# Optimization experiments

Measured on AMD Instinct MI355X. Metric: run time of the kernel, lower is better.

Reference implementation:

```python
import jax, jax.numpy as jnp
import numpy as np
from jax import lax

B, N, C_IN = 8, 4096, 64
NPOINT, NSAMPLE, RADIUS = 1024, 32, 0.2
BN_EPS = 1e-3  # keras BatchNormalization default epsilon


def _fps(pts):
    """Farthest point sampling on a single cloud pts: (N, 3) -> (NPOINT,) int32."""
    n = pts.shape[0]
    def step(carry, _):
        dist, far = carry
        c = pts[far]                                  # (3,)
        d = jnp.sum((pts - c) ** 2, axis=-1)          # (N,)
        dist = jnp.minimum(dist, d)
        nxt = jnp.argmax(dist).astype(jnp.int32)
        return (dist, nxt), far
    init = (jnp.full((n,), 1e10, pts.dtype), jnp.array(0, jnp.int32))
    _, idx = lax.scan(step, init, None, length=NPOINT)
    return idx


def _ball_query(xyz, new_xyz):
    """xyz: (B,N,3), new_xyz: (B,P,3) -> idx (B,P,NSAMPLE) int32.
    First NSAMPLE point indices within RADIUS of each centroid (in original
    order); slots beyond the in-ball count are filled with the first in-ball
    index, matching the PointNet++ CUDA query_ball_point semantics."""
    n = xyz.shape[1]
    # squared distances via the expansion trick to avoid a (B,P,N,3) temp
    d2 = (jnp.sum(new_xyz ** 2, -1)[:, :, None]
          + jnp.sum(xyz ** 2, -1)[:, None, :]
          - 2.0 * jnp.einsum('bpc,bnc->bpn', new_xyz, xyz))  # (B,P,N)
    in_ball = d2 < RADIUS ** 2
    cand = jnp.where(in_ball, jnp.arange(n, dtype=jnp.int32)[None, None, :], n)
    neg_top, _ = lax.top_k(-cand, NSAMPLE)   # NSAMPLE smallest indices
    idx = -neg_top                           # ascending order
    first = idx[..., :1]                     # centroid itself is always in-ball
    idx = jnp.where(idx == n, first, idx)
    return idx


def _group(feats, idx):
    """feats: (B,N,C), idx: (B,P,S) -> (B,P,S,C) gather per batch."""
    return jax.vmap(lambda f, i: f[i])(feats, idx)


def _mlp_layer(x, W, g, b, m, v):
    # 1x1 conv (no bias) + BN (inference stats) + ReLU
    x = jnp.einsum('bpsc,cd->bpsd', x, W)
    x = (x - m) * lax.rsqrt(v + BN_EPS) * g + b
    return jax.nn.relu(x)


def setup_inputs() -> dict:
    key = jax.random.key(0)
    ks = jax.random.split(key, 8)
    xyz = jax.random.uniform(ks[0], (B, N, 3), dtype=jnp.float32)
    points = jax.random.normal(ks[1], (B, N, C_IN), dtype=jnp.float32)
    c0 = 3 + C_IN  # use_xyz=True
    W0 = jax.random.normal(ks[2], (c0, 64), jnp.float32) / np.sqrt(c0)
    W1 = jax.random.normal(ks[3], (64, 64), jnp.float32) / np.sqrt(64.0)
    W2 = jax.random.normal(ks[4], (64, 128), jnp.float32) / np.sqrt(64.0)
    def bn(c):
        return (jnp.ones((c,), jnp.float32), jnp.zeros((c,), jnp.float32),
                jnp.zeros((c,), jnp.float32), jnp.ones((c,), jnp.float32))
    g0, b0, m0, v0 = bn(64)
    g1, b1, m1, v1 = bn(64)
    g2, b2, m2, v2 = bn(128)
    return dict(xyz=xyz, points=points,
                W0=W0, g0=g0, b0=b0, m0=m0, v0=v0,
                W1=W1, g1=g1, b1=b1, m1=m1, v1=v1,
                W2=W2, g2=g2, b2=b2, m2=m2, v2=v2)


def reference(xyz, points,
              W0, g0, b0, m0, v0,
              W1, g1, b1, m1, v1,
              W2, g2, b2, m2, v2):
    # --- sample_and_group ---
    fps_idx = jax.vmap(_fps)(xyz)                            # (B,P)
    new_xyz = jnp.take_along_axis(xyz, fps_idx[:, :, None], axis=1)  # (B,P,3)
    idx = _ball_query(xyz, new_xyz)                          # (B,P,S)
    grouped_xyz = _group(xyz, idx) - new_xyz[:, :, None, :]  # (B,P,S,3)
    grouped_pts = _group(points, idx)                        # (B,P,S,C)
    new_points = jnp.concatenate([grouped_xyz, grouped_pts], axis=-1)
    # --- shared per-point MLP (1x1 conv + BN + ReLU) ---
    new_points = _mlp_layer(new_points, W0, g0, b0, m0, v0)
    new_points = _mlp_layer(new_points, W1, g1, b1, m1, v1)
    new_points = _mlp_layer(new_points, W2, g2, b2, m2, v2)
    # --- max pool over the neighborhood axis ---
    new_points = jnp.max(new_points, axis=2)                 # (B,P,128)
    return new_xyz, new_points, idx
```

## Files before the change

kernel.cpp:

```cpp
#include <hip/hip_runtime.h>
#include <stdint.h>

#define BN_EPS 0.001f

typedef float v2f __attribute__((ext_vector_type(2)));

__global__ __launch_bounds__(256) void fps_kernel(const float* __restrict__ xyz,
                                                  float* __restrict__ new_xyz) {
#pragma clang fp contract(off)
  __shared__ float px[4096], py[4096], pz[4096];
  __shared__ unsigned long long wk[2][4];
  __shared__ int curh[1024];
  const int b = blockIdx.x;
  const int t = threadIdx.x;
  const int lane = t & 63, wid = t >> 6;
  const float* X = xyz + (size_t)b * 4096 * 3;
  v2f x[8], y[8], z[8], dist[8];
#pragma unroll
  for (int j = 0; j < 8; ++j) {
    const int n0 = (2 * j) * 256 + t;
    const int n1 = (2 * j + 1) * 256 + t;
    x[j].x = X[n0 * 3 + 0]; x[j].y = X[n1 * 3 + 0];
    y[j].x = X[n0 * 3 + 1]; y[j].y = X[n1 * 3 + 1];
    z[j].x = X[n0 * 3 + 2]; z[j].y = X[n1 * 3 + 2];
    px[n0] = x[j].x; py[n0] = y[j].x; pz[n0] = z[j].x;
    px[n1] = x[j].y; py[n1] = y[j].y; pz[n1] = z[j].y;
    dist[j] = (v2f){1e10f, 1e10f};
  }
  __syncthreads();
  int cur = 0;
  for (int it = 0; it < 1024; ++it) {
    if (t == 0) curh[it] = cur;
    const float cx = px[cur], cy = py[cur], cz = pz[cur];
    const v2f cxv = {cx, cx}, cyv = {cy, cy}, czv = {cz, cz};
    float bestv = -1.0f;
    int bestj = 0;
#pragma unroll
    for (int j = 0; j < 8; ++j) {
      v2f dx = x[j] - cxv, dy = y[j] - cyv, dz = z[j] - czv;
      v2f d = dx * dx + dy * dy;
      d = d + dz * dz;
      v2f nd = __builtin_elementwise_min(dist[j], d);
      dist[j] = nd;
      if (nd.x > bestv) { bestv = nd.x; bestj = 2 * j; }
      if (nd.y > bestv) { bestv = nd.y; bestj = 2 * j + 1; }
    }
    const int besti = bestj * 256 + t;
    unsigned long long key =
        ((unsigned long long)__float_as_uint(bestv) << 32) | (unsigned)(~besti);
#define DPP_STEP(CTRL)                                                                     \
    {                                                                                      \
      unsigned lo_ = (unsigned)key, hi_ = (unsigned)(key >> 32);                           \
      unsigned ls = (unsigned)__builtin_amdgcn_update_dpp((int)lo_, (int)lo_, CTRL, 0xf, 0xf, false); \
      unsigned hs = (unsigned)__builtin_amdgcn_update_dpp((int)hi_, (int)hi_, CTRL, 0xf, 0xf, false); \
      unsigned long long sk = ((unsigned long long)hs << 32) | ls;                         \
      if (sk > key) key = sk;                                                              \
    }
    DPP_STEP(0x111)
    DPP_STEP(0x112)
    DPP_STEP(0x114)
    DPP_STEP(0x118)
    DPP_STEP(0x142)
    DPP_STEP(0x143)
#undef DPP_STEP
    const unsigned whi = (unsigned)__builtin_amdgcn_readlane((int)(key >> 32), 63);
    const unsigned wlo = (unsigned)__builtin_amdgcn_readlane((int)key, 63);
    if (lane == 0) wk[it & 1][wid] = ((unsigned long long)whi << 32) | wlo;
    __syncthreads();
    const unsigned long long k0 = wk[it & 1][0], k1 = wk[it & 1][1];
    const unsigned long long k2 = wk[it & 1][2], k3 = wk[it & 1][3];
    unsigned long long b01 = (k1 > k0) ? k1 : k0;
    unsigned long long b23 = (k3 > k2) ? k3 : k2;
    unsigned long long bk = (b23 > b01) ? b23 : b01;
    cur = (int)(~(unsigned)(bk & 0xffffffffull));
  }
  __syncthreads();
  float* out = new_xyz + (size_t)b * 1024 * 3;
  for (int it = t; it < 1024; it += 256) {
    const int c = curh[it];
    out[it * 3 + 0] = px[c];
    out[it * 3 + 1] = py[c];
    out[it * 3 + 2] = pz[c];
  }
}

__global__ __launch_bounds__(256) void ballq_kernel(const float* __restrict__ xyz,
                                                    const float* __restrict__ new_xyz,
                                                    float* __restrict__ idxf) {
#pragma clang fp contract(off)
  const int wv = threadIdx.x >> 6, lane = threadIdx.x & 63;
  const int pg = blockIdx.x * 4 + wv;
  const int b = pg >> 10;
  const float* X = xyz + (size_t)b * 4096 * 3;
  const float cx = new_xyz[pg * 3 + 0];
  const float cy = new_xyz[pg * 3 + 1];
  const float cz = new_xyz[pg * 3 + 2];
  const float csq = (cx * cx + cy * cy) + cz * cz;
  float* out = idxf + (size_t)pg * 32;
  int total = 0;
  int first = -1;
  for (int chunk = 0; chunk < 64; ++chunk) {
    const int n = chunk * 64 + lane;
    const float xx = X[n * 3 + 0], yy = X[n * 3 + 1], zz = X[n * 3 + 2];
    const float sq = (xx * xx + yy * yy) + zz * zz;
    const float dot = fmaf(cz, zz, fmaf(cy, yy, cx * xx));
    const float d2 = (csq + sq) - 2.0f * dot;
    const bool in = d2 < 0.04f;
    const unsigned long long mask = __ballot(in);
    if (first < 0 && mask != 0ull) first = chunk * 64 + __builtin_ctzll(mask);
    if (in) {
      const int pos = total + __builtin_popcountll(mask & ((1ull << lane) - 1ull));
      if (pos < 32) out[pos] = (float)n;
    }
    total += __builtin_popcountll(mask);
    if (total >= 32) break;
  }
  if (total < 32 && first >= 0) {
    const int slot = total + lane;
    if (slot < 32) out[slot] = (float)first;
  }
}

__global__ __launch_bounds__(256) void mlp_kernel(
    const float* __restrict__ xyz, const float* __restrict__ points,
    const float* __restrict__ new_xyz, const float* __restrict__ idxf,
    const float* __restrict__ W0, const float* __restrict__ g0,
    const float* __restrict__ b0, const float* __restrict__ m0,
    const float* __restrict__ v0, const float* __restrict__ W1,
    const float* __restrict__ g1, const float* __restrict__ b1,
    const float* __restrict__ m1, const float* __restrict__ v1,
    const float* __restrict__ W2, const float* __restrict__ g2,
    const float* __restrict__ b2, const float* __restrict__ m2,
    const float* __restrict__ v2, float* __restrict__ new_points) {
  __shared__ __align__(16) float W0s[67 * 64];
  __shared__ __align__(16) float W1s[64 * 64];
  __shared__ __align__(16) float sh[64 * 36];
  __shared__ __align__(16) float h0T[64 * 34];
  __shared__ float s0c[64], t0c[64], s1c[64], t1c[64], s2c[128], t2c[128];
  const int t = threadIdx.x;
  float* inT = sh;
  float* h1T = sh;

  for (int i = t; i < 67 * 64; i += 256) W0s[i] = W0[i];
  for (int i = t; i < 64 * 64; i += 256) W1s[i] = W1[i];
  if (t < 64) {
    float s = g0[t] * rsqrtf(v0[t] + BN_EPS); s0c[t] = s; t0c[t] = b0[t] - m0[t] * s;
    float u = g1[t] * rsqrtf(v1[t] + BN_EPS); s1c[t] = u; t1c[t] = b1[t] - m1[t] * u;
  }
  if (t < 128) {
    float s = g2[t] * rsqrtf(v2[t] + BN_EPS); s2c[t] = s; t2c[t] = b2[t] - m2[t] * s;
  }
  __syncthreads();

  const int sgrp = t & 15, dgrp = t >> 4;
  const int dg2 = t & 31, sg2 = t >> 5;
  float* pmax = h0T;

  for (int pp = 0; pp < 4; ++pp) {
    const int pg = blockIdx.x * 4 + pp;
    const int b = pg >> 10;
    const float cx = new_xyz[pg * 3 + 0];
    const float cy = new_xyz[pg * 3 + 1];
    const float cz = new_xyz[pg * 3 + 2];
    {
      const int s = t >> 3, cg = t & 7;
      const int i = (int)idxf[(size_t)pg * 32 + s];
      const float* Pr = points + ((size_t)b * 4096 + i) * 64 + cg * 8;
      const float4 a = *(const float4*)Pr;
      const float4 c4 = *(const float4*)(Pr + 4);
      const int r = 3 + cg * 8;
      inT[(r + 0) * 34 + s] = a.x;  inT[(r + 1) * 34 + s] = a.y;
      inT[(r + 2) * 34 + s] = a.z;  inT[(r + 3) * 34 + s] = a.w;
      inT[(r + 4) * 34 + s] = c4.x; inT[(r + 5) * 34 + s] = c4.y;
      inT[(r + 6) * 34 + s] = c4.z; inT[(r + 7) * 34 + s] = c4.w;
      if (t < 32) {
        const int i2 = (int)idxf[(size_t)pg * 32 + t];
        const float* Xr = xyz + ((size_t)b * 4096 + i2) * 3;
        inT[0 * 34 + t] = Xr[0] - cx;
        inT[1 * 34 + t] = Xr[1] - cy;
        inT[2 * 34 + t] = Xr[2] - cz;
      }
    }
    __syncthreads();
    {
      float acc[2][4] = {{0, 0, 0, 0}, {0, 0, 0, 0}};
#pragma unroll 4
      for (int c = 0; c < 67; ++c) {
        const float2 a = *(const float2*)&inT[c * 34 + 2 * sgrp];
        const float4 w = *(const float4*)&W0s[c * 64 + 4 * dgrp];
        acc[0][0] = fmaf(a.x, w.x, acc[0][0]); acc[0][1] = fmaf(a.x, w.y, acc[0][1]);
        acc[0][2] = fmaf(a.x, w.z, acc[0][2]); acc[0][3] = fmaf(a.x, w.w, acc[0][3]);
        acc[1][0] = fmaf(a.y, w.x, acc[1][0]); acc[1][1] = fmaf(a.y, w.y, acc[1][1]);
        acc[1][2] = fmaf(a.y, w.z, acc[1][2]); acc[1][3] = fmaf(a.y, w.w, acc[1][3]);
      }
#pragma unroll
      for (int dj = 0; dj < 4; ++dj) {
        const int d = 4 * dgrp + dj;
        const float s = s0c[d], bb = t0c[d];
#pragma unroll
        for (int si = 0; si < 2; ++si) {
          float yv = fmaf(acc[si][dj], s, bb);
          h0T[d * 34 + 2 * sgrp + si] = fmaxf(yv, 0.0f);
        }
      }
    }
    __syncthreads();
    {
      float acc[2][4] = {{0, 0, 0, 0}, {0, 0, 0, 0}};
#pragma unroll 4
      for (int c = 0; c < 64; ++c) {
        const float2 a = *(const float2*)&h0T[c * 34 + 2 * sgrp];
        const float4 w = *(const float4*)&W1s[c * 64 + 4 * dgrp];
        acc[0][0] = fmaf(a.x, w.x, acc[0][0]); acc[0][1] = fmaf(a.x, w.y, acc[0][1]);
        acc[0][2] = fmaf(a.x, w.z, acc[0][2]); acc[0][3] = fmaf(a.x, w.w, acc[0][3]);
        acc[1][0] = fmaf(a.y, w.x, acc[1][0]); acc[1][1] = fmaf(a.y, w.y, acc[1][1]);
        acc[1][2] = fmaf(a.y, w.z, acc[1][2]); acc[1][3] = fmaf(a.y, w.w, acc[1][3]);
      }
#pragma unroll
      for (int dj = 0; dj < 4; ++dj) {
        const int d = 4 * dgrp + dj;
        const float s = s1c[d], bb = t1c[d];
#pragma unroll
        for (int si = 0; si < 2; ++si) {
          float yv = fmaf(acc[si][dj], s, bb);
          h1T[d * 36 + 2 * sgrp + si] = fmaxf(yv, 0.0f);
        }
      }
    }
    __syncthreads();
    {
      float acc[4][4] = {{0,0,0,0},{0,0,0,0},{0,0,0,0},{0,0,0,0}};
#pragma unroll 8
      for (int c = 0; c < 64; ++c) {
        const float4 a = *(const float4*)&h1T[c * 36 + 4 * sg2];
        const float4 w = *(const float4*)(W2 + c * 128 + 4 * dg2);
        acc[0][0] = fmaf(a.x, w.x, acc[0][0]); acc[0][1] = fmaf(a.x, w.y, acc[0][1]);
        acc[0][2] = fmaf(a.x, w.z, acc[0][2]); acc[0][3] = fmaf(a.x, w.w, acc[0][3]);
        acc[1][0] = fmaf(a.y, w.x, acc[1][0]); acc[1][1] = fmaf(a.y, w.y, acc[1][1]);
        acc[1][2] = fmaf(a.y, w.z, acc[1][2]); acc[1][3] = fmaf(a.y, w.w, acc[1][3]);
        acc[2][0] = fmaf(a.z, w.x, acc[2][0]); acc[2][1] = fmaf(a.z, w.y, acc[2][1]);
        acc[2][2] = fmaf(a.z, w.z, acc[2][2]); acc[2][3] = fmaf(a.z, w.w, acc[2][3]);
        acc[3][0] = fmaf(a.w, w.x, acc[3][0]); acc[3][1] = fmaf(a.w, w.y, acc[3][1]);
        acc[3][2] = fmaf(a.w, w.z, acc[3][2]); acc[3][3] = fmaf(a.w, w.w, acc[3][3]);
      }
#pragma unroll
      for (int dj = 0; dj < 4; ++dj) {
        const int d = 4 * dg2 + dj;
        const float s = s2c[d], bb = t2c[d];
        float mx = 0.0f;
#pragma unroll
        for (int si = 0; si < 4; ++si) {
          float yv = fmaf(acc[si][dj], s, bb);
          mx = fmaxf(mx, fmaxf(yv, 0.0f));
        }
        pmax[sg2 * 128 + d] = mx;
      }
    }
    __syncthreads();
    if (t < 128) {
      float mx = pmax[t];
#pragma unroll
      for (int g = 1; g < 8; ++g) mx = fmaxf(mx, pmax[g * 128 + t]);
      new_points[(size_t)pg * 128 + t] = mx;
    }
    __syncthreads();
  }
}

extern "C" void kernel_launch(void* const* d_in, const int* in_sizes, int n_in,
                              void* d_out, int out_size, void* d_ws, size_t ws_size,
                              hipStream_t stream) {
  (void)in_sizes; (void)n_in; (void)out_size; (void)d_ws; (void)ws_size;
  const float* xyz    = (const float*)d_in[0];
  const float* points = (const float*)d_in[1];
  const float* W0 = (const float*)d_in[2];
  const float* g0 = (const float*)d_in[3];
  const float* b0 = (const float*)d_in[4];
  const float* m0 = (const float*)d_in[5];
  const float* v0 = (const float*)d_in[6];
  const float* W1 = (const float*)d_in[7];
  const float* g1 = (const float*)d_in[8];
  const float* b1 = (const float*)d_in[9];
  const float* m1 = (const float*)d_in[10];
  const float* v1 = (const float*)d_in[11];
  const float* W2 = (const float*)d_in[12];
  const float* g2 = (const float*)d_in[13];
  const float* b2 = (const float*)d_in[14];
  const float* m2 = (const float*)d_in[15];
  const float* v2 = (const float*)d_in[16];

  float* new_xyz    = (float*)d_out;
  float* new_points = new_xyz + 8 * 1024 * 3;
  float* idxf       = new_points + 8 * 1024 * 128;

  fps_kernel<<<8, 256, 0, stream>>>(xyz, new_xyz);
  ballq_kernel<<<2048, 256, 0, stream>>>(xyz, new_xyz, idxf);
  mlp_kernel<<<2048, 256, 0, stream>>>(xyz, points, new_xyz, idxf,
                                       W0, g0, b0, m0, v0,
                                       W1, g1, b1, m1, v1,
                                       W2, g2, b2, m2, v2, new_points);
}
```

Baseline: 821.8 us.

## Fuse FPS, ball query and MLP into one persistent kernel with progress flags

Merges the three kernels into a single persistent launch. Eight blocks run farthest point sampling and publish centroids in chunks of 32 through release-stored progress counters. The remaining 256 blocks spin on those counters and run ball query plus the MLP for each group of four centroids as soon as they are ready. Ball-query indices are also kept in shared memory so they need not be reread from global. The aim is to overlap the long serial FPS phase with downstream work, at the cost of spin-waiting, a memset launch, and reliance on all 264 blocks being co-resident.

```diff
diff --git a/kernel.cpp b/kernel.cpp
--- a/kernel.cpp
+++ b/kernel.cpp
@@ -5,125 +5,30 @@
 
 typedef float v2f __attribute__((ext_vector_type(2)));
 
-__global__ __launch_bounds__(256) void fps_kernel(const float* __restrict__ xyz,
-                                                  float* __restrict__ new_xyz) {
-#pragma clang fp contract(off)
-  __shared__ float px[4096], py[4096], pz[4096];
-  __shared__ unsigned long long wk[2][4];
-  __shared__ int curh[1024];
-  const int b = blockIdx.x;
-  const int t = threadIdx.x;
-  const int lane = t & 63, wid = t >> 6;
-  const float* X = xyz + (size_t)b * 4096 * 3;
-  v2f x[8], y[8], z[8], dist[8];
-#pragma unroll
-  for (int j = 0; j < 8; ++j) {
-    const int n0 = (2 * j) * 256 + t;
-    const int n1 = (2 * j + 1) * 256 + t;
-    x[j].x = X[n0 * 3 + 0]; x[j].y = X[n1 * 3 + 0];
-    y[j].x = X[n0 * 3 + 1]; y[j].y = X[n1 * 3 + 1];
-    z[j].x = X[n0 * 3 + 2]; z[j].y = X[n1 * 3 + 2];
-    px[n0] = x[j].x; py[n0] = y[j].x; pz[n0] = z[j].x;
-    px[n1] = x[j].y; py[n1] = y[j].y; pz[n1] = z[j].y;
-    dist[j] = (v2f){1e10f, 1e10f};
-  }
-  __syncthreads();
-  int cur = 0;
-  for (int it = 0; it < 1024; ++it) {
-    if (t == 0) curh[it] = cur;
-    const float cx = px[cur], cy = py[cur], cz = pz[cur];
-    const v2f cxv = {cx, cx}, cyv = {cy, cy}, czv = {cz, cz};
-    float bestv = -1.0f;
-    int bestj = 0;
-#pragma unroll
-    for (int j = 0; j < 8; ++j) {
-      v2f dx = x[j] - cxv, dy = y[j] - cyv, dz = z[j] - czv;
-      v2f d = dx * dx + dy * dy;
-      d = d + dz * dz;
-      v2f nd = __builtin_elementwise_min(dist[j], d);
-      dist[j] = nd;
-      if (nd.x > bestv) { bestv = nd.x; bestj = 2 * j; }
-      if (nd.y > bestv) { bestv = nd.y; bestj = 2 * j + 1; }
-    }
-    const int besti = bestj * 256 + t;
-    unsigned long long key =
-        ((unsigned long long)__float_as_uint(bestv) << 32) | (unsigned)(~besti);
-#define DPP_STEP(CTRL)                                                                     \
-    {                                                                                      \
-      unsigned lo_ = (unsigned)key, hi_ = (unsigned)(key >> 32);                           \
-      unsigned ls = (unsigned)__builtin_amdgcn_update_dpp((int)lo_, (int)lo_, CTRL, 0xf, 0xf, false); \
-      unsigned hs = (unsigned)__builtin_amdgcn_update_dpp((int)hi_, (int)hi_, CTRL, 0xf, 0xf, false); \
-      unsigned long long sk = ((unsigned long long)hs << 32) | ls;                         \
-      if (sk > key) key = sk;                                                              \
-    }
-    DPP_STEP(0x111)
-    DPP_STEP(0x112)
-    DPP_STEP(0x114)
-    DPP_STEP(0x118)
-    DPP_STEP(0x142)
-    DPP_STEP(0x143)
-#undef DPP_STEP
-    const unsigned whi = (unsigned)__builtin_amdgcn_readlane((int)(key >> 32), 63);
-    const unsigned wlo = (unsigned)__builtin_amdgcn_readlane((int)key, 63);
-    if (lane == 0) wk[it & 1][wid] = ((unsigned long long)whi << 32) | wlo;
-    __syncthreads();
-    const unsigned long long k0 = wk[it & 1][0], k1 = wk[it & 1][1];
-    const unsigned long long k2 = wk[it & 1][2], k3 = wk[it & 1][3];
-    unsigned long long b01 = (k1 > k0) ? k1 : k0;
-    unsigned long long b23 = (k3 > k2) ? k3 : k2;
-    unsigned long long bk = (b23 > b01) ? b23 : b01;
-    cur = (int)(~(unsigned)(bk & 0xffffffffull));
-  }
-  __syncthreads();
-  float* out = new_xyz + (size_t)b * 1024 * 3;
-  for (int it = t; it < 1024; it += 256) {
-    const int c = curh[it];
-    out[it * 3 + 0] = px[c];
-    out[it * 3 + 1] = py[c];
-    out[it * 3 + 2] = pz[c];
-  }
-}
-
-__global__ __launch_bounds__(256) void ballq_kernel(const float* __restrict__ xyz,
-                                                    const float* __restrict__ new_xyz,
-                                                    float* __restrict__ idxf) {
-#pragma clang fp contract(off)
-  const int wv = threadIdx.x >> 6, lane = threadIdx.x & 63;
-  const int pg = blockIdx.x * 4 + wv;
-  const int b = pg >> 10;
-  const float* X = xyz + (size_t)b * 4096 * 3;
-  const float cx = new_xyz[pg * 3 + 0];
-  const float cy = new_xyz[pg * 3 + 1];
-  const float cz = new_xyz[pg * 3 + 2];
-  const float csq = (cx * cx + cy * cy) + cz * cz;
-  float* out = idxf + (size_t)pg * 32;
-  int total = 0;
-  int first = -1;
-  for (int chunk = 0; chunk < 64; ++chunk) {
-    const int n = chunk * 64 + lane;
-    const float xx = X[n * 3 + 0], yy = X[n * 3 + 1], zz = X[n * 3 + 2];
-    const float sq = (xx * xx + yy * yy) + zz * zz;
-    const float dot = fmaf(cz, zz, fmaf(cy, yy, cx * xx));
-    const float d2 = (csq + sq) - 2.0f * dot;
-    const bool in = d2 < 0.04f;
-    const unsigned long long mask = __ballot(in);
-    if (first < 0 && mask != 0ull) first = chunk * 64 + __builtin_ctzll(mask);
-    if (in) {
-      const int pos = total + __builtin_popcountll(mask & ((1ull << lane) - 1ull));
-      if (pos < 32) out[pos] = (float)n;
-    }
-    total += __builtin_popcountll(mask);
-    if (total >= 32) break;
-  }
-  if (total < 32 && first >= 0) {
-    const int slot = total + lane;
-    if (slot < 32) out[slot] = (float)first;
-  }
-}
-
-__global__ __launch_bounds__(256) void mlp_kernel(
+
+struct FpsSh {
+  float px[4096], py[4096], pz[4096];
+  unsigned long long wk[2][4];
+  int curh[32];
+};
+
+struct WrkSh {
+  float W0s[67 * 64];
+  float W1s[64 * 64];
+  float sh[64 * 36];
+  float h0T[64 * 34];
+  float s0c[64], t0c[64], s1c[64], t1c[64], s2c[128], t2c[128];
+  float idxs[4 * 32];
+  float cent[4 * 3];
+};
+
+union AllSh {
+  FpsSh f;
+  WrkSh w;
+};
+
+__global__ __launch_bounds__(256) void fused_kernel(
     const float* __restrict__ xyz, const float* __restrict__ points,
-    const float* __restrict__ new_xyz, const float* __restrict__ idxf,
     const float* __restrict__ W0, const float* __restrict__ g0,
     const float* __restrict__ b0, const float* __restrict__ m0,
     const float* __restrict__ v0, const float* __restrict__ W1,
@@ -131,16 +36,105 @@
     const float* __restrict__ m1, const float* __restrict__ v1,
     const float* __restrict__ W2, const float* __restrict__ g2,
     const float* __restrict__ b2, const float* __restrict__ m2,
-    const float* __restrict__ v2, float* __restrict__ new_points) {
-  __shared__ __align__(16) float W0s[67 * 64];
-  __shared__ __align__(16) float W1s[64 * 64];
-  __shared__ __align__(16) float sh[64 * 36];
-  __shared__ __align__(16) float h0T[64 * 34];
-  __shared__ float s0c[64], t0c[64], s1c[64], t1c[64], s2c[128], t2c[128];
+    const float* __restrict__ v2, float* __restrict__ new_xyz,
+    float* __restrict__ new_points, float* __restrict__ idxf,
+    unsigned int* __restrict__ prog) {
+  __shared__ __align__(16) AllSh smem;
+  const int bid = blockIdx.x;
   const int t = threadIdx.x;
-  float* inT = sh;
-  float* h1T = sh;
-
+
+  if (bid < 8) {
+#pragma clang fp contract(off)
+    float* px = smem.f.px;
+    float* py = smem.f.py;
+    float* pz = smem.f.pz;
+    int* curh = smem.f.curh;
+    auto& wk = smem.f.wk;
+    const int lane = t & 63, wid = t >> 6;
+    const int b = bid;
+    const float* X = xyz + (size_t)b * 4096 * 3;
+    float* out = new_xyz + (size_t)b * 1024 * 3;
+    v2f x[8], y[8], z[8], dist[8];
+#pragma unroll
+    for (int j = 0; j < 8; ++j) {
+      const int n0 = (2 * j) * 256 + t;
+      const int n1 = (2 * j + 1) * 256 + t;
+      x[j].x = X[n0 * 3 + 0]; x[j].y = X[n1 * 3 + 0];
+      y[j].x = X[n0 * 3 + 1]; y[j].y = X[n1 * 3 + 1];
+      z[j].x = X[n0 * 3 + 2]; z[j].y = X[n1 * 3 + 2];
+      px[n0] = x[j].x; py[n0] = y[j].x; pz[n0] = z[j].x;
+      px[n1] = x[j].y; py[n1] = y[j].y; pz[n1] = z[j].y;
+      dist[j] = (v2f){1e10f, 1e10f};
+    }
+    __syncthreads();
+    int cur = 0;
+    for (int cc = 0; cc < 32; ++cc) {
+      for (int ii = 0; ii < 32; ++ii) {
+        const int it = cc * 32 + ii;
+        if (t == 0) curh[ii] = cur;
+        const float cx = px[cur], cy = py[cur], cz = pz[cur];
+        const v2f cxv = {cx, cx}, cyv = {cy, cy}, czv = {cz, cz};
+        float bestv = -1.0f;
+        int bestj = 0;
+#pragma unroll
+        for (int j = 0; j < 8; ++j) {
+          v2f dx = x[j] - cxv, dy = y[j] - cyv, dz = z[j] - czv;
+          v2f d = dx * dx + dy * dy;
+          d = d + dz * dz;
+          v2f nd = __builtin_elementwise_min(dist[j], d);
+          dist[j] = nd;
+          if (nd.x > bestv) { bestv = nd.x; bestj = 2 * j; }
+          if (nd.y > bestv) { bestv = nd.y; bestj = 2 * j + 1; }
+        }
+        const int besti = bestj * 256 + t;
+        unsigned long long key =
+            ((unsigned long long)__float_as_uint(bestv) << 32) | (unsigned)(~besti);
+#define DPP_STEP(CTRL)                                                                     \
+        {                                                                                  \
+          unsigned lo_ = (unsigned)key, hi_ = (unsigned)(key >> 32);                       \
+          unsigned ls = (unsigned)__builtin_amdgcn_update_dpp((int)lo_, (int)lo_, CTRL, 0xf, 0xf, false); \
+          unsigned hs = (unsigned)__builtin_amdgcn_update_dpp((int)hi_, (int)hi_, CTRL, 0xf, 0xf, false); \
+          unsigned long long sk = ((unsigned long long)hs << 32) | ls;                     \
+          if (sk > key) key = sk;                                                          \
+        }
+        DPP_STEP(0x111)
+        DPP_STEP(0x112)
+        DPP_STEP(0x114)
+        DPP_STEP(0x118)
+        DPP_STEP(0x142)
+        DPP_STEP(0x143)
+#undef DPP_STEP
+        const unsigned whi = (unsigned)__builtin_amdgcn_readlane((int)(key >> 32), 63);
+        const unsigned wlo = (unsigned)__builtin_amdgcn_readlane((int)key, 63);
+        if (lane == 0) wk[it & 1][wid] = ((unsigned long long)whi << 32) | wlo;
+        __syncthreads();
+        const unsigned long long k0 = wk[it & 1][0], k1 = wk[it & 1][1];
+        const unsigned long long k2 = wk[it & 1][2], k3 = wk[it & 1][3];
+        unsigned long long b01 = (k1 > k0) ? k1 : k0;
+        unsigned long long b23 = (k3 > k2) ? k3 : k2;
+        unsigned long long bk = (b23 > b01) ? b23 : b01;
+        cur = (int)(~(unsigned)(bk & 0xffffffffull));
+      }
+      if (t < 32) {
+        const int c = curh[t];
+        const int p = cc * 32 + t;
+        out[p * 3 + 0] = px[c];
+        out[p * 3 + 1] = py[c];
+        out[p * 3 + 2] = pz[c];
+      }
+      __syncthreads();
+      if (t == 0)
+        __hip_atomic_store(&prog[b * 32], (unsigned)(cc * 32 + 32),
+                           __ATOMIC_RELEASE, __HIP_MEMORY_SCOPE_AGENT);
+    }
+    return;
+  }
+
+  float* W0s = smem.w.W0s;
+  float* W1s = smem.w.W1s;
+  float* s0c = smem.w.s0c; float* t0c = smem.w.t0c;
+  float* s1c = smem.w.s1c; float* t1c = smem.w.t1c;
+  float* s2c = smem.w.s2c; float* t2c = smem.w.t2c;
   for (int i = t; i < 67 * 64; i += 256) W0s[i] = W0[i];
   for (int i = t; i < 64 * 64; i += 256) W1s[i] = W1[i];
   if (t < 64) {
@@ -151,126 +145,186 @@
     float s = g2[t] * rsqrtf(v2[t] + BN_EPS); s2c[t] = s; t2c[t] = b2[t] - m2[t] * s;
   }
   __syncthreads();
-
   const int sgrp = t & 15, dgrp = t >> 4;
   const int dg2 = t & 31, sg2 = t >> 5;
+  float* inT = smem.w.sh;
+  float* h1T = smem.w.sh;
+  float* h0T = smem.w.h0T;
   float* pmax = h0T;
 
-  for (int pp = 0; pp < 4; ++pp) {
-    const int pg = blockIdx.x * 4 + pp;
-    const int b = pg >> 10;
-    const float cx = new_xyz[pg * 3 + 0];
-    const float cy = new_xyz[pg * 3 + 1];
-    const float cz = new_xyz[pg * 3 + 2];
+  int kbeg, kend, kstep;
+  if (bid >= 256) { kbeg = 2032 + (bid - 256); kend = 2048; kstep = 8; }
+  else            { kbeg = bid - 8;            kend = 2032; kstep = 248; }
+
+  for (int k = kbeg; k < kend; k += kstep) {
+    const int j = k >> 3, b = k & 7;
+    const int pgbase = b * 1024 + j * 4;
+    const unsigned need = (unsigned)(j * 4 + 4);
     {
-      const int s = t >> 3, cg = t & 7;
-      const int i = (int)idxf[(size_t)pg * 32 + s];
-      const float* Pr = points + ((size_t)b * 4096 + i) * 64 + cg * 8;
-      const float4 a = *(const float4*)Pr;
-      const float4 c4 = *(const float4*)(Pr + 4);
-      const int r = 3 + cg * 8;
-      inT[(r + 0) * 34 + s] = a.x;  inT[(r + 1) * 34 + s] = a.y;
-      inT[(r + 2) * 34 + s] = a.z;  inT[(r + 3) * 34 + s] = a.w;
-      inT[(r + 4) * 34 + s] = c4.x; inT[(r + 5) * 34 + s] = c4.y;
-      inT[(r + 6) * 34 + s] = c4.z; inT[(r + 7) * 34 + s] = c4.w;
-      if (t < 32) {
-        const int i2 = (int)idxf[(size_t)pg * 32 + t];
-        const float* Xr = xyz + ((size_t)b * 4096 + i2) * 3;
-        inT[0 * 34 + t] = Xr[0] - cx;
-        inT[1 * 34 + t] = Xr[1] - cy;
-        inT[2 * 34 + t] = Xr[2] - cz;
+      int guard = 0;
+      while (__hip_atomic_load(&prog[b * 32], __ATOMIC_RELAXED,
+                               __HIP_MEMORY_SCOPE_AGENT) < need) {
+        __builtin_amdgcn_s_sleep(32);
+        if (++guard > (1 << 20)) break;
+      }
+      (void)__hip_atomic_load(&prog[b * 32], __ATOMIC_ACQUIRE,
+                              __HIP_MEMORY_SCOPE_AGENT);
+    }
+    {
+#pragma clang fp contract(off)
+      const int wv = t >> 6, lane = t & 63;
+      const int pg = pgbase + wv;
+      const float* X = xyz + (size_t)b * 4096 * 3;
+      const float cx = new_xyz[pg * 3 + 0];
+      const float cy = new_xyz[pg * 3 + 1];
+      const float cz = new_xyz[pg * 3 + 2];
+      const float csq = (cx * cx + cy * cy) + cz * cz;
+      float* outg = idxf + (size_t)pg * 32;
+      float* ol = smem.w.idxs + wv * 32;
+      int total = 0;
+      int first = -1;
+      for (int chunk = 0; chunk < 64; ++chunk) {
+        const int n = chunk * 64 + lane;
+        const float xx = X[n * 3 + 0], yy = X[n * 3 + 1], zz = X[n * 3 + 2];
+        const float sq = (xx * xx + yy * yy) + zz * zz;
+        const float dot = fmaf(cz, zz, fmaf(cy, yy, cx * xx));
+        const float d2 = (csq + sq) - 2.0f * dot;
+        const bool in = d2 < 0.04f;
+        const unsigned long long mask = __ballot(in);
+        if (first < 0 && mask != 0ull) first = chunk * 64 + __builtin_ctzll(mask);
+        if (in) {
+          const int pos = total + __builtin_popcountll(mask & ((1ull << lane) - 1ull));
+          if (pos < 32) { outg[pos] = (float)n; ol[pos] = (float)n; }
+        }
+        total += __builtin_popcountll(mask);
+        if (total >= 32) break;
+      }
+      if (total < 32 && first >= 0) {
+        const int slot = total + lane;
+        if (slot < 32) { outg[slot] = (float)first; ol[slot] = (float)first; }
+      }
+      if (lane == 0) {
+        smem.w.cent[wv * 3 + 0] = cx;
+        smem.w.cent[wv * 3 + 1] = cy;
+        smem.w.cent[wv * 3 + 2] = cz;
       }
     }
     __syncthreads();
-    {
-      float acc[2][4] = {{0, 0, 0, 0}, {0, 0, 0, 0}};
+    for (int pp = 0; pp < 4; ++pp) {
+      const int pg = pgbase + pp;
+      const float cx = smem.w.cent[pp * 3 + 0];
+      const float cy = smem.w.cent[pp * 3 + 1];
+      const float cz = smem.w.cent[pp * 3 + 2];
+      {
+        const int s = t >> 3, cg = t & 7;
+        const int i = (int)smem.w.idxs[pp * 32 + s];
+        const float* Pr = points + ((size_t)b * 4096 + i) * 64 + cg * 8;
+        const float4 a = *(const float4*)Pr;
+        const float4 c4 = *(const float4*)(Pr + 4);
+        const int r = 3 + cg * 8;
+        inT[(r + 0) * 34 + s] = a.x;  inT[(r + 1) * 34 + s] = a.y;
+        inT[(r + 2) * 34 + s] = a.z;  inT[(r + 3) * 34 + s] = a.w;
+        inT[(r + 4) * 34 + s] = c4.x; inT[(r + 5) * 34 + s] = c4.y;
+        inT[(r + 6) * 34 + s] = c4.z; inT[(r + 7) * 34 + s] = c4.w;
+        if (t < 32) {
+          const int i2 = (int)smem.w.idxs[pp * 32 + t];
+          const float* Xr = xyz + ((size_t)b * 4096 + i2) * 3;
+          inT[0 * 34 + t] = Xr[0] - cx;
+          inT[1 * 34 + t] = Xr[1] - cy;
+          inT[2 * 34 + t] = Xr[2] - cz;
+        }
+      }
+      __syncthreads();
+      {
+        float acc[2][4] = {{0, 0, 0, 0}, {0, 0, 0, 0}};
 #pragma unroll 4
-      for (int c = 0; c < 67; ++c) {
-        const float2 a = *(const float2*)&inT[c * 34 + 2 * sgrp];
-        const float4 w = *(const float4*)&W0s[c * 64 + 4 * dgrp];
-        acc[0][0] = fmaf(a.x, w.x, acc[0][0]); acc[0][1] = fmaf(a.x, w.y, acc[0][1]);
-        acc[0][2] = fmaf(a.x, w.z, acc[0][2]); acc[0][3] = fmaf(a.x, w.w, acc[0][3]);
-        acc[1][0] = fmaf(a.y, w.x, acc[1][0]); acc[1][1] = fmaf(a.y, w.y, acc[1][1]);
-        acc[1][2] = fmaf(a.y, w.z, acc[1][2]); acc[1][3] = fmaf(a.y, w.w, acc[1][3]);
-      }
-#pragma unroll
-      for (int dj = 0; dj < 4; ++dj) {
-        const int d = 4 * dgrp + dj;
-        const float s = s0c[d], bb = t0c[d];
-#pragma unroll
-        for (int si = 0; si < 2; ++si) {
-          float yv = fmaf(acc[si][dj], s, bb);
-          h0T[d * 34 + 2 * sgrp + si] = fmaxf(yv, 0.0f);
-        }
-      }
-    }
-    __syncthreads();
-    {
-      float acc[2][4] = {{0, 0, 0, 0}, {0, 0, 0, 0}};
+        for (int c = 0; c < 67; ++c) {
+          const float2 a = *(const float2*)&inT[c * 34 + 2 * sgrp];
+          const float4 w = *(const float4*)&W0s[c * 64 + 4 * dgrp];
+          acc[0][0] = fmaf(a.x, w.x, acc[0][0]); acc[0][1] = fmaf(a.x, w.y, acc[0][1]);
+          acc[0][2] = fmaf(a.x, w.z, acc[0][2]); acc[0][3] = fmaf(a.x, w.w, acc[0][3]);
+          acc[1][0] = fmaf(a.y, w.x, acc[1][0]); acc[1][1] = fmaf(a.y, w.y, acc[1][1]);
+          acc[1][2] = fmaf(a.y, w.z, acc[1][2]); acc[1][3] = fmaf(a.y, w.w, acc[1][3]);
+        }
+#pragma unroll
+        for (int dj = 0; dj < 4; ++dj) {
+          const int d = 4 * dgrp + dj;
+          const float s = s0c[d], bb = t0c[d];
+#pragma unroll
+          for (int si = 0; si < 2; ++si) {
+            float yv = fmaf(acc[si][dj], s, bb);
+            h0T[d * 34 + 2 * sgrp + si] = fmaxf(yv, 0.0f);
+          }
+        }
+      }
+      __syncthreads();
+      {
+        float acc[2][4] = {{0, 0, 0, 0}, {0, 0, 0, 0}};
 #pragma unroll 4
-      for (int c = 0; c < 64; ++c) {
-        const float2 a = *(const float2*)&h0T[c * 34 + 2 * sgrp];
-        const float4 w = *(const float4*)&W1s[c * 64 + 4 * dgrp];
-        acc[0][0] = fmaf(a.x, w.x, acc[0][0]); acc[0][1] = fmaf(a.x, w.y, acc[0][1]);
-        acc[0][2] = fmaf(a.x, w.z, acc[0][2]); acc[0][3] = fmaf(a.x, w.w, acc[0][3]);
-        acc[1][0] = fmaf(a.y, w.x, acc[1][0]); acc[1][1] = fmaf(a.y, w.y, acc[1][1]);
-        acc[1][2] = fmaf(a.y, w.z, acc[1][2]); acc[1][3] = fmaf(a.y, w.w, acc[1][3]);
-      }
-#pragma unroll
-      for (int dj = 0; dj < 4; ++dj) {
-        const int d = 4 * dgrp + dj;
-        const float s = s1c[d], bb = t1c[d];
-#pragma unroll
-        for (int si = 0; si < 2; ++si) {
-          float yv = fmaf(acc[si][dj], s, bb);
-          h1T[d * 36 + 2 * sgrp + si] = fmaxf(yv, 0.0f);
-        }
-      }
-    }
-    __syncthreads();
-    {
-      float acc[4][4] = {{0,0,0,0},{0,0,0,0},{0,0,0,0},{0,0,0,0}};
+        for (int c = 0; c < 64; ++c) {
+          const float2 a = *(const float2*)&h0T[c * 34 + 2 * sgrp];
+          const float4 w = *(const float4*)&W1s[c * 64 + 4 * dgrp];
+          acc[0][0] = fmaf(a.x, w.x, acc[0][0]); acc[0][1] = fmaf(a.x, w.y, acc[0][1]);
+          acc[0][2] = fmaf(a.x, w.z, acc[0][2]); acc[0][3] = fmaf(a.x, w.w, acc[0][3]);
+          acc[1][0] = fmaf(a.y, w.x, acc[1][0]); acc[1][1] = fmaf(a.y, w.y, acc[1][1]);
+          acc[1][2] = fmaf(a.y, w.z, acc[1][2]); acc[1][3] = fmaf(a.y, w.w, acc[1][3]);
+        }
+#pragma unroll
+        for (int dj = 0; dj < 4; ++dj) {
+          const int d = 4 * dgrp + dj;
+          const float s = s1c[d], bb = t1c[d];
+#pragma unroll
+          for (int si = 0; si < 2; ++si) {
+            float yv = fmaf(acc[si][dj], s, bb);
+            h1T[d * 36 + 2 * sgrp + si] = fmaxf(yv, 0.0f);
+          }
+        }
+      }
+      __syncthreads();
+      {
+        float acc[4][4] = {{0,0,0,0},{0,0,0,0},{0,0,0,0},{0,0,0,0}};
 #pragma unroll 8
-      for (int c = 0; c < 64; ++c) {
-        const float4 a = *(const float4*)&h1T[c * 36 + 4 * sg2];
-        const float4 w = *(const float4*)(W2 + c * 128 + 4 * dg2);
-        acc[0][0] = fmaf(a.x, w.x, acc[0][0]); acc[0][1] = fmaf(a.x, w.y, acc[0][1]);
-        acc[0][2] = fmaf(a.x, w.z, acc[0][2]); acc[0][3] = fmaf(a.x, w.w, acc[0][3]);
-        acc[1][0] = fmaf(a.y, w.x, acc[1][0]); acc[1][1] = fmaf(a.y, w.y, acc[1][1]);
-        acc[1][2] = fmaf(a.y, w.z, acc[1][2]); acc[1][3] = fmaf(a.y, w.w, acc[1][3]);
-        acc[2][0] = fmaf(a.z, w.x, acc[2][0]); acc[2][1] = fmaf(a.z, w.y, acc[2][1]);
-        acc[2][2] = fmaf(a.z, w.z, acc[2][2]); acc[2][3] = fmaf(a.z, w.w, acc[2][3]);
-        acc[3][0] = fmaf(a.w, w.x, acc[3][0]); acc[3][1] = fmaf(a.w, w.y, acc[3][1]);
-        acc[3][2] = fmaf(a.w, w.z, acc[3][2]); acc[3][3] = fmaf(a.w, w.w, acc[3][3]);
-      }
-#pragma unroll
-      for (int dj = 0; dj < 4; ++dj) {
-        const int d = 4 * dg2 + dj;
-        const float s = s2c[d], bb = t2c[d];
-        float mx = 0.0f;
-#pragma unroll
-        for (int si = 0; si < 4; ++si) {
-          float yv = fmaf(acc[si][dj], s, bb);
-          mx = fmaxf(mx, fmaxf(yv, 0.0f));
-        }
-        pmax[sg2 * 128 + d] = mx;
-      }
-    }
-    __syncthreads();
-    if (t < 128) {
-      float mx = pmax[t];
-#pragma unroll
-      for (int g = 1; g < 8; ++g) mx = fmaxf(mx, pmax[g * 128 + t]);
-      new_points[(size_t)pg * 128 + t] = mx;
-    }
-    __syncthreads();
+        for (int c = 0; c < 64; ++c) {
+          const float4 a = *(const float4*)&h1T[c * 36 + 4 * sg2];
+          const float4 w = *(const float4*)(W2 + c * 128 + 4 * dg2);
+          acc[0][0] = fmaf(a.x, w.x, acc[0][0]); acc[0][1] = fmaf(a.x, w.y, acc[0][1]);
+          acc[0][2] = fmaf(a.x, w.z, acc[0][2]); acc[0][3] = fmaf(a.x, w.w, acc[0][3]);
+          acc[1][0] = fmaf(a.y, w.x, acc[1][0]); acc[1][1] = fmaf(a.y, w.y, acc[1][1]);
+          acc[1][2] = fmaf(a.y, w.z, acc[1][2]); acc[1][3] = fmaf(a.y, w.w, acc[1][3]);
+          acc[2][0] = fmaf(a.z, w.x, acc[2][0]); acc[2][1] = fmaf(a.z, w.y, acc[2][1]);
+          acc[2][2] = fmaf(a.z, w.z, acc[2][2]); acc[2][3] = fmaf(a.z, w.w, acc[2][3]);
+          acc[3][0] = fmaf(a.w, w.x, acc[3][0]); acc[3][1] = fmaf(a.w, w.y, acc[3][1]);
+          acc[3][2] = fmaf(a.w, w.z, acc[3][2]); acc[3][3] = fmaf(a.w, w.w, acc[3][3]);
+        }
+#pragma unroll
+        for (int dj = 0; dj < 4; ++dj) {
+          const int d = 4 * dg2 + dj;
+          const float s = s2c[d], bb = t2c[d];
+          float mx = 0.0f;
+#pragma unroll
+          for (int si = 0; si < 4; ++si) {
+            float yv = fmaf(acc[si][dj], s, bb);
+            mx = fmaxf(mx, fmaxf(yv, 0.0f));
+          }
+          pmax[sg2 * 128 + d] = mx;
+        }
+      }
+      __syncthreads();
+      if (t < 128) {
+        float mx = pmax[t];
+#pragma unroll
+        for (int g = 1; g < 8; ++g) mx = fmaxf(mx, pmax[g * 128 + t]);
+        new_points[(size_t)pg * 128 + t] = mx;
+      }
+      __syncthreads();
+    }
   }
 }
 
 extern "C" void kernel_launch(void* const* d_in, const int* in_sizes, int n_in,
                               void* d_out, int out_size, void* d_ws, size_t ws_size,
                               hipStream_t stream) {
-  (void)in_sizes; (void)n_in; (void)out_size; (void)d_ws; (void)ws_size;
+  (void)in_sizes; (void)n_in; (void)out_size; (void)ws_size;
   const float* xyz    = (const float*)d_in[0];
   const float* points = (const float*)d_in[1];
   const float* W0 = (const float*)d_in[2];
@@ -293,10 +347,10 @@
   float* new_points = new_xyz + 8 * 1024 * 3;
   float* idxf       = new_points + 8 * 1024 * 128;
 
-  fps_kernel<<<8, 256, 0, stream>>>(xyz, new_xyz);
-  ballq_kernel<<<2048, 256, 0, stream>>>(xyz, new_xyz, idxf);
-  mlp_kernel<<<2048, 256, 0, stream>>>(xyz, points, new_xyz, idxf,
-                                       W0, g0, b0, m0, v0,
-                                       W1, g1, b1, m1, v1,
-                                       W2, g2, b2, m2, v2, new_points);
+  unsigned int* prog = (unsigned int*)d_ws;
+  hipMemsetAsync(d_ws, 0, 8 * 32 * sizeof(unsigned int), stream);
+  fused_kernel<<<264, 256, 0, stream>>>(xyz, points, W0, g0, b0, m0, v0,
+                                        W1, g1, b1, m1, v1,
+                                        W2, g2, b2, m2, v2,
+                                        new_xyz, new_points, idxf, prog);
 }
```

Measured after the change: 780.4 us. -5.0%, faster.
